# Kernel tuning notes

Hardware: AMD Instinct MI355X
Metric: run time of the kernel (lower is better)

The kernel has to match this reference:

```python
import jax, jax.numpy as jnp
import numpy as np

N = 100000     # nodes
E = 1600000    # directed edges
IN, HID, OUT = 128, 64, 64


def setup_inputs() -> dict:
    key = jax.random.key(0)
    k = jax.random.split(key, 6)
    features = jax.random.normal(k[0], (N, IN), dtype=jnp.float32)
    edge_index = jax.random.randint(k[1], (2, E), 0, N, dtype=jnp.int64)
    # Glorot-ish init for linear weights, zeros for bias (PyG GCNConv default)
    W1 = jax.random.normal(k[2], (IN, HID), dtype=jnp.float32) / np.sqrt(IN)
    b1 = jnp.zeros((HID,), dtype=jnp.float32)
    W2 = jax.random.normal(k[3], (HID, OUT), dtype=jnp.float32) / np.sqrt(HID)
    b2 = jnp.zeros((OUT,), dtype=jnp.float32)
    return {"features": features, "edge_index": edge_index, "batch_size": N,
            "W1": W1, "b1": b1, "W2": W2, "b2": b2}


def _gcn_conv(x, W, b, src, dst, n):
    """PyG GCNConv: add self-loops, symmetric deg^-1/2 normalization,
    linear transform then scatter-add aggregation, plus bias."""
    loops = jnp.arange(n, dtype=src.dtype)
    s = jnp.concatenate([src, loops])   # [E+N]
    d = jnp.concatenate([dst, loops])   # [E+N]
    deg = jax.ops.segment_sum(jnp.ones(s.shape, dtype=x.dtype), d, num_segments=n)
    dinv = jnp.where(deg > 0, jax.lax.rsqrt(deg), jnp.zeros_like(deg))
    norm = dinv[s] * dinv[d]            # [E+N]
    h = x @ W                           # [n, out] transform before aggregation
    msg = h[s] * norm[:, None]          # gather + scale  [E+N, out]
    out = jax.ops.segment_sum(msg, d, num_segments=n)  # scatter-add
    return out + b


def reference(features, edge_index, batch_size, W1, b1, W2, b2):
    src, dst = edge_index[0], edge_index[1]
    n = features.shape[0]
    x = _gcn_conv(features, W1, b1, src, dst, n)
    x = jax.nn.relu(x)
    # F.dropout(training=self.training): module is in eval mode -> identity
    x = _gcn_conv(x, W2, b2, src, dst, n)
    return jax.nn.log_softmax(x, axis=1)
```

## Files before the change

### kernel.cpp

```cpp
#include <hip/hip_runtime.h>
#include <math.h>

#define K1 128
#define C  64
#define SCAN_B 1024

__global__ void detect_kernel(const int* __restrict__ e, int twoE, int* __restrict__ flag) {
    __shared__ int nz;
    if (threadIdx.x == 0) nz = 0;
    __syncthreads();
    int nchk = twoE / 2; if (nchk > 4096) nchk = 4096;
    int bad = 0;
    for (int i = threadIdx.x; i < nchk; i += blockDim.x)
        if (e[2 * i + 1] != 0) bad = 1;
    if (bad) atomicOr(&nz, 1);
    __syncthreads();
    if (threadIdx.x == 0) *flag = nz ? 0 : 1;
}

__global__ void convert_kernel(const void* __restrict__ ein, int twoE,
                               const int* __restrict__ flag, int* __restrict__ eout) {
    int is64 = *flag;
    int i = blockIdx.x * blockDim.x + threadIdx.x;
    int stride = gridDim.x * blockDim.x;
    if (is64) {
        const long long* p = (const long long*)ein;
        for (; i < twoE; i += stride) eout[i] = (int)p[i];
    } else {
        const int* p = (const int*)ein;
        for (; i < twoE; i += stride) eout[i] = p[i];
    }
}

__global__ void zero_kernel(int* __restrict__ p, int n) {
    for (int i = blockIdx.x * blockDim.x + threadIdx.x; i < n; i += gridDim.x * blockDim.x)
        p[i] = 0;
}

__global__ void cnt_kernel(const int* __restrict__ dst, int E, int* __restrict__ cnt) {
    for (int e = blockIdx.x * blockDim.x + threadIdx.x; e < E; e += gridDim.x * blockDim.x)
        atomicAdd(&cnt[dst[e]], 1);
}

__global__ void dinv_kernel(const int* __restrict__ cnt, float* __restrict__ dinv, int n) {
    for (int i = blockIdx.x * blockDim.x + threadIdx.x; i < n; i += gridDim.x * blockDim.x)
        dinv[i] = rsqrtf((float)(cnt[i] + 1));
}

__global__ __launch_bounds__(SCAN_B) void scan1_kernel(const int* __restrict__ cnt, int n,
        int* __restrict__ ex, int* __restrict__ bsum) {
    __shared__ int s[SCAN_B];
    int i = blockIdx.x * SCAN_B + threadIdx.x;
    int v = (i < n) ? cnt[i] : 0;
    s[threadIdx.x] = v;
    __syncthreads();
    for (int off = 1; off < SCAN_B; off <<= 1) {
        int t = (threadIdx.x >= off) ? s[threadIdx.x - off] : 0;
        __syncthreads();
        s[threadIdx.x] += t;
        __syncthreads();
    }
    if (i < n) ex[i] = s[threadIdx.x] - v;
    if (threadIdx.x == SCAN_B - 1) bsum[blockIdx.x] = s[SCAN_B - 1];
}

__global__ void scan2_kernel(int* __restrict__ bsum, int nb) {
    const int lane = threadIdx.x & 63;
    int acc = 0;
    for (int base = 0; base < nb; base += 64) {
        int v = (base + lane < nb) ? bsum[base + lane] : 0;
        int sc = v;
        #pragma unroll
        for (int off = 1; off < 64; off <<= 1) {
            int t = __shfl_up(sc, off, 64);
            if (lane >= off) sc += t;
        }
        if (base + lane < nb) bsum[base + lane] = acc + sc - v;
        acc += __shfl(sc, 63, 64);
    }
}

__global__ void scan3_kernel(int* __restrict__ ex, const int* __restrict__ bsum,
                             int* __restrict__ fill, int n, int Etot) {
    for (int i = blockIdx.x * blockDim.x + threadIdx.x; i < n; i += gridDim.x * blockDim.x) {
        int v = ex[i] + bsum[i / SCAN_B];
        ex[i] = v;
        fill[i] = v;
    }
    if (blockIdx.x == 0 && threadIdx.x == 0) ex[n] = Etot;
}

__global__ void scatter_kernel(const int* __restrict__ src, const int* __restrict__ dst,
                               int E, int* __restrict__ fill, int* __restrict__ csr) {
    for (int e = blockIdx.x * blockDim.x + threadIdx.x; e < E; e += gridDim.x * blockDim.x) {
        int pos = atomicAdd(&fill[dst[e]], 1);
        csr[pos] = src[e];
    }
}

template<int K, int R>
__global__ __launch_bounds__(256) void gemm_kernel(const float* __restrict__ X,
        const float* __restrict__ W, const float* __restrict__ dinv,
        float* __restrict__ G, int n)
{
    __shared__ float Ws[K * C];
    for (int i = threadIdx.x; i < K * C; i += 256) Ws[i] = W[i];
    __syncthreads();
    const int lane = threadIdx.x & 63;
    const int wave = __builtin_amdgcn_readfirstlane((int)(threadIdx.x >> 6));
    const int waves = gridDim.x * 4;
    for (int base = (blockIdx.x * 4 + wave) * R; base < n; base += waves * R) {
        float acc[R];
        #pragma unroll
        for (int r = 0; r < R; ++r) acc[r] = 0.0f;
        if (base + R <= n) {
            for (int k = 0; k < K; ++k) {
                float w = Ws[k * C + lane];
                #pragma unroll
                for (int r = 0; r < R; ++r)
                    acc[r] = fmaf(X[(size_t)(base + r) * K + k], w, acc[r]);
            }
            #pragma unroll
            for (int r = 0; r < R; ++r)
                G[(size_t)(base + r) * C + lane] = acc[r] * dinv[base + r];
        } else {
            for (int r = 0; r < R; ++r) {
                if (base + r >= n) break;
                float a = 0.0f;
                for (int k = 0; k < K; ++k)
                    a = fmaf(X[(size_t)(base + r) * K + k], Ws[k * C + lane], a);
                G[(size_t)(base + r) * C + lane] = a * dinv[base + r];
            }
        }
    }
}

template<int MODE>
__global__ __launch_bounds__(256) void gather_kernel(const int* __restrict__ rowptr,
        const int* __restrict__ csr, const float* __restrict__ G,
        const float* __restrict__ dinv, const float* __restrict__ bias,
        float* __restrict__ Out, int n)
{
    const int lane = threadIdx.x & 63;
    const int v = __builtin_amdgcn_readfirstlane((int)(blockIdx.x * 4 + (threadIdx.x >> 6)));
    if (v >= n) return;
    const int start = __builtin_amdgcn_readfirstlane(rowptr[v]);
    const int end   = __builtin_amdgcn_readfirstlane(rowptr[v + 1]);
    float a0 = G[(size_t)v * C + lane];
    float a1 = 0.f, a2 = 0.f, a3 = 0.f;
    for (int base = start; base < end; base += 64) {
        int m = end - base; if (m > 64) m = 64;
        int idx = (lane < m) ? csr[base + lane] : 0;
        int j = 0;
        for (; j + 4 <= m; j += 4) {
            int s0 = __shfl(idx, j,     64);
            int s1 = __shfl(idx, j + 1, 64);
            int s2 = __shfl(idx, j + 2, 64);
            int s3 = __shfl(idx, j + 3, 64);
            a0 += G[(size_t)s0 * C + lane];
            a1 += G[(size_t)s1 * C + lane];
            a2 += G[(size_t)s2 * C + lane];
            a3 += G[(size_t)s3 * C + lane];
        }
        for (; j < m; ++j) {
            int s = __shfl(idx, j, 64);
            a0 += G[(size_t)s * C + lane];
        }
    }
    float acc = (a0 + a1) + (a2 + a3);
    float y = fmaf(acc, dinv[v], bias[lane]);
    if (MODE == 0) {
        Out[(size_t)v * C + lane] = y > 0.f ? y : 0.f;
    } else {
        float mx = y;
        #pragma unroll
        for (int off = 32; off > 0; off >>= 1) mx = fmaxf(mx, __shfl_xor(mx, off, 64));
        float ex = expf(y - mx);
        float l = ex;
        #pragma unroll
        for (int off = 32; off > 0; off >>= 1) l += __shfl_xor(l, off, 64);
        Out[(size_t)v * C + lane] = y - mx - logf(l);
    }
}

static inline size_t align16(size_t x) { return (x + 15) & ~(size_t)15; }

extern "C" void kernel_launch(void* const* d_in, const int* in_sizes, int n_in,
                              void* d_out, int out_size, void* d_ws, size_t ws_size,
                              hipStream_t stream)
{
    const float* X  = (const float*)d_in[0];
    const void*  EI = d_in[1];
    const float* W1 = (const float*)d_in[3];
    const float* b1 = (const float*)d_in[4];
    const float* W2 = (const float*)d_in[5];
    const float* b2 = (const float*)d_in[6];
    float* Out = (float*)d_out;

    const int n    = in_sizes[0] / K1;
    const int E    = in_sizes[1] / 2;
    const int twoE = 2 * E;
    const int nb   = (n + SCAN_B - 1) / SCAN_B;

    char* ws = (char*)d_ws;
    size_t off = 0;
    int*   edges  = (int*)(ws + off); off = align16(off + (size_t)twoE * 4);
    int*   csr    = (int*)(ws + off); off = align16(off + (size_t)E * 4);
    int*   rowptr = (int*)(ws + off); off = align16(off + (size_t)(n + 1) * 4);
    int*   cnt    = (int*)(ws + off); off = align16(off + (size_t)n * 4);
    int*   bsum   = (int*)(ws + off); off = align16(off + (size_t)(nb + 1) * 4);
    int*   flag   = (int*)(ws + off); off = align16(off + 16);
    float* dinv   = (float*)(ws + off); off = align16(off + (size_t)n * 4);
    float* G      = (float*)(ws + off); off = align16(off + (size_t)n * C * 4);
    int*   fill   = cnt;
    float* H      = Out;

    const int* srcp = edges;
    const int* dstp = edges + E;

    hipLaunchKernelGGL(detect_kernel,  dim3(1),    dim3(256), 0, stream, (const int*)EI, twoE, flag);
    hipLaunchKernelGGL(convert_kernel, dim3(4096), dim3(256), 0, stream, EI, twoE, flag, edges);

    hipLaunchKernelGGL(zero_kernel, dim3(512),  dim3(256), 0, stream, cnt, n);
    hipLaunchKernelGGL(cnt_kernel,  dim3(2048), dim3(256), 0, stream, dstp, E, cnt);
    hipLaunchKernelGGL(dinv_kernel, dim3(512),  dim3(256), 0, stream, cnt, dinv, n);
    hipLaunchKernelGGL(scan1_kernel, dim3(nb), dim3(SCAN_B), 0, stream, cnt, n, rowptr, bsum);
    hipLaunchKernelGGL(scan2_kernel, dim3(1),  dim3(64),     0, stream, bsum, nb);
    hipLaunchKernelGGL(scan3_kernel, dim3(1024), dim3(256),  0, stream, rowptr, bsum, fill, n, E);
    hipLaunchKernelGGL(scatter_kernel, dim3(2048), dim3(256), 0, stream, srcp, dstp, E, fill, csr);

    const int ngb = (n + 3) / 4;

    hipLaunchKernelGGL((gemm_kernel<K1, 8>), dim3(2048), dim3(256), 0, stream, X, W1, dinv, G, n);
    hipLaunchKernelGGL((gather_kernel<0>), dim3(ngb), dim3(256), 0, stream, rowptr, csr, G, dinv, b1, H, n);

    hipLaunchKernelGGL((gemm_kernel<C, 8>), dim3(2048), dim3(256), 0, stream, H, W2, dinv, G, n);
    hipLaunchKernelGGL((gather_kernel<1>), dim3(ngb), dim3(256), 0, stream, rowptr, csr, G, dinv, b2, Out, n);
}
```

Before: 583.4 us.

## Fuse layer-2 GEMM into gather, store features in fp16, drop edge conversion

Removes the edge int64-to-int32 conversion pass by reading edge_index directly in the histogram and scatter kernels. The degree-inverse computation moves into the scan kernel, and a memset replaces the zero kernel. The transformed features G are now stored as fp16, halving the bytes moved by the random-gather aggregation. The layer-1 aggregation is fused with ReLU and the layer-2 64x64 transform, which drops a full GEMM pass and the H round-trip, at the cost of 64 registers of W2 per thread and reduced-precision intermediates.

```diff
diff --git a/kernel.cpp b/kernel.cpp
--- a/kernel.cpp
+++ b/kernel.cpp
@@ -1,4 +1,5 @@
 #include <hip/hip_runtime.h>
+#include <hip/hip_fp16.h>
 #include <math.h>
 
 #define K1 128
@@ -18,37 +19,22 @@
     if (threadIdx.x == 0) *flag = nz ? 0 : 1;
 }
 
-__global__ void convert_kernel(const void* __restrict__ ein, int twoE,
-                               const int* __restrict__ flag, int* __restrict__ eout) {
-    int is64 = *flag;
-    int i = blockIdx.x * blockDim.x + threadIdx.x;
-    int stride = gridDim.x * blockDim.x;
-    if (is64) {
-        const long long* p = (const long long*)ein;
-        for (; i < twoE; i += stride) eout[i] = (int)p[i];
-    } else {
-        const int* p = (const int*)ein;
-        for (; i < twoE; i += stride) eout[i] = p[i];
-    }
-}
-
-__global__ void zero_kernel(int* __restrict__ p, int n) {
-    for (int i = blockIdx.x * blockDim.x + threadIdx.x; i < n; i += gridDim.x * blockDim.x)
-        p[i] = 0;
-}
-
-__global__ void cnt_kernel(const int* __restrict__ dst, int E, int* __restrict__ cnt) {
-    for (int e = blockIdx.x * blockDim.x + threadIdx.x; e < E; e += gridDim.x * blockDim.x)
-        atomicAdd(&cnt[dst[e]], 1);
-}
-
-__global__ void dinv_kernel(const int* __restrict__ cnt, float* __restrict__ dinv, int n) {
-    for (int i = blockIdx.x * blockDim.x + threadIdx.x; i < n; i += gridDim.x * blockDim.x)
-        dinv[i] = rsqrtf((float)(cnt[i] + 1));
+__device__ __forceinline__ int load_dst(const void* EI, int E, int e, int is64) {
+    return is64 ? (int)((const long long*)EI)[(size_t)E + e] : ((const int*)EI)[(size_t)E + e];
+}
+__device__ __forceinline__ int load_src(const void* EI, int E, int e, int is64) {
+    return is64 ? (int)((const long long*)EI)[e] : ((const int*)EI)[e];
+}
+
+__global__ __launch_bounds__(256) void hist_kernel(const void* __restrict__ EI, int E,
+        const int* __restrict__ flag, int* __restrict__ cnt) {
+    const int is64 = *flag;
+    for (int e = blockIdx.x * 256 + threadIdx.x; e < E; e += gridDim.x * 256)
+        atomicAdd(&cnt[load_dst(EI, E, e, is64)], 1);
 }
 
 __global__ __launch_bounds__(SCAN_B) void scan1_kernel(const int* __restrict__ cnt, int n,
-        int* __restrict__ ex, int* __restrict__ bsum) {
+        int* __restrict__ ex, int* __restrict__ bsum, float* __restrict__ dinv) {
     __shared__ int s[SCAN_B];
     int i = blockIdx.x * SCAN_B + threadIdx.x;
     int v = (i < n) ? cnt[i] : 0;
@@ -60,7 +46,10 @@
         s[threadIdx.x] += t;
         __syncthreads();
     }
-    if (i < n) ex[i] = s[threadIdx.x] - v;
+    if (i < n) {
+        ex[i] = s[threadIdx.x] - v;
+        dinv[i] = rsqrtf((float)(v + 1));
+    }
     if (threadIdx.x == SCAN_B - 1) bsum[blockIdx.x] = s[SCAN_B - 1];
 }
 
@@ -90,18 +79,21 @@
     if (blockIdx.x == 0 && threadIdx.x == 0) ex[n] = Etot;
 }
 
-__global__ void scatter_kernel(const int* __restrict__ src, const int* __restrict__ dst,
-                               int E, int* __restrict__ fill, int* __restrict__ csr) {
-    for (int e = blockIdx.x * blockDim.x + threadIdx.x; e < E; e += gridDim.x * blockDim.x) {
-        int pos = atomicAdd(&fill[dst[e]], 1);
-        csr[pos] = src[e];
+__global__ __launch_bounds__(256) void scatter_kernel(const void* __restrict__ EI, int E,
+        const int* __restrict__ flag, int* __restrict__ fill, int* __restrict__ csr) {
+    const int is64 = *flag;
+    for (int e = blockIdx.x * 256 + threadIdx.x; e < E; e += gridDim.x * 256) {
+        int d = load_dst(EI, E, e, is64);
+        int s = load_src(EI, E, e, is64);
+        int pos = atomicAdd(&fill[d], 1);
+        csr[pos] = s;
     }
 }
 
 template<int K, int R>
 __global__ __launch_bounds__(256) void gemm_kernel(const float* __restrict__ X,
         const float* __restrict__ W, const float* __restrict__ dinv,
-        float* __restrict__ G, int n)
+        __half* __restrict__ G, int n)
 {
     __shared__ float Ws[K * C];
     for (int i = threadIdx.x; i < K * C; i += 256) Ws[i] = W[i];
@@ -122,22 +114,74 @@
             }
             #pragma unroll
             for (int r = 0; r < R; ++r)
-                G[(size_t)(base + r) * C + lane] = acc[r] * dinv[base + r];
+                G[(size_t)(base + r) * C + lane] = __float2half_rn(acc[r] * dinv[base + r]);
         } else {
             for (int r = 0; r < R; ++r) {
                 if (base + r >= n) break;
                 float a = 0.0f;
                 for (int k = 0; k < K; ++k)
                     a = fmaf(X[(size_t)(base + r) * K + k], Ws[k * C + lane], a);
-                G[(size_t)(base + r) * C + lane] = a * dinv[base + r];
-            }
-        }
-    }
-}
-
-template<int MODE>
-__global__ __launch_bounds__(256) void gather_kernel(const int* __restrict__ rowptr,
-        const int* __restrict__ csr, const float* __restrict__ G,
+                G[(size_t)(base + r) * C + lane] = __float2half_rn(a * dinv[base + r]);
+            }
+        }
+    }
+}
+
+__global__ __launch_bounds__(256) void gather_fused_kernel(const int* __restrict__ rowptr,
+        const int* __restrict__ csr, const __half* __restrict__ G,
+        const float* __restrict__ dinv, const float* __restrict__ b1,
+        const float* __restrict__ W2, __half* __restrict__ G2, int n)
+{
+    __shared__ __align__(16) float Hrow[4][C];
+    const int lane = threadIdx.x & 63;
+    const int wv = __builtin_amdgcn_readfirstlane((int)(threadIdx.x >> 6));
+    float w[C];
+    #pragma unroll
+    for (int k = 0; k < C; ++k) w[k] = W2[k * C + lane];
+    const float bias = b1[lane];
+    const int nwaves = gridDim.x * 4;
+    for (int v = __builtin_amdgcn_readfirstlane(blockIdx.x * 4 + wv); v < n; v += nwaves) {
+        const int start = __builtin_amdgcn_readfirstlane(rowptr[v]);
+        const int end   = __builtin_amdgcn_readfirstlane(rowptr[v + 1]);
+        float a0 = __half2float(G[(size_t)v * C + lane]);
+        float a1 = 0.f, a2 = 0.f, a3 = 0.f;
+        for (int base = start; base < end; base += 64) {
+            int m = end - base; if (m > 64) m = 64;
+            int idx = (lane < m) ? csr[base + lane] : 0;
+            int j = 0;
+            for (; j + 4 <= m; j += 4) {
+                int s0 = __shfl(idx, j,     64);
+                int s1 = __shfl(idx, j + 1, 64);
+                int s2 = __shfl(idx, j + 2, 64);
+                int s3 = __shfl(idx, j + 3, 64);
+                a0 += __half2float(G[(size_t)s0 * C + lane]);
+                a1 += __half2float(G[(size_t)s1 * C + lane]);
+                a2 += __half2float(G[(size_t)s2 * C + lane]);
+                a3 += __half2float(G[(size_t)s3 * C + lane]);
+            }
+            for (; j < m; ++j) {
+                int s = __shfl(idx, j, 64);
+                a0 += __half2float(G[(size_t)s * C + lane]);
+            }
+        }
+        float y = fmaf((a0 + a1) + (a2 + a3), dinv[v], bias);
+        y = y > 0.f ? y : 0.f;
+        Hrow[wv][lane] = y;
+        float o = 0.f;
+        #pragma unroll
+        for (int k0 = 0; k0 < C / 4; ++k0) {
+            float4 h4 = *(const float4*)&Hrow[wv][k0 * 4];
+            o = fmaf(h4.x, w[4 * k0 + 0], o);
+            o = fmaf(h4.y, w[4 * k0 + 1], o);
+            o = fmaf(h4.z, w[4 * k0 + 2], o);
+            o = fmaf(h4.w, w[4 * k0 + 3], o);
+        }
+        G2[(size_t)v * C + lane] = __float2half_rn(o * dinv[v]);
+    }
+}
+
+__global__ __launch_bounds__(256) void gather_ls_kernel(const int* __restrict__ rowptr,
+        const int* __restrict__ csr, const __half* __restrict__ G,
         const float* __restrict__ dinv, const float* __restrict__ bias,
         float* __restrict__ Out, int n)
 {
@@ -146,7 +190,7 @@
     if (v >= n) return;
     const int start = __builtin_amdgcn_readfirstlane(rowptr[v]);
     const int end   = __builtin_amdgcn_readfirstlane(rowptr[v + 1]);
-    float a0 = G[(size_t)v * C + lane];
+    float a0 = __half2float(G[(size_t)v * C + lane]);
     float a1 = 0.f, a2 = 0.f, a3 = 0.f;
     for (int base = start; base < end; base += 64) {
         int m = end - base; if (m > 64) m = 64;
@@ -157,30 +201,25 @@
             int s1 = __shfl(idx, j + 1, 64);
             int s2 = __shfl(idx, j + 2, 64);
             int s3 = __shfl(idx, j + 3, 64);
-            a0 += G[(size_t)s0 * C + lane];
-            a1 += G[(size_t)s1 * C + lane];
-            a2 += G[(size_t)s2 * C + lane];
-            a3 += G[(size_t)s3 * C + lane];
+            a0 += __half2float(G[(size_t)s0 * C + lane]);
+            a1 += __half2float(G[(size_t)s1 * C + lane]);
+            a2 += __half2float(G[(size_t)s2 * C + lane]);
+            a3 += __half2float(G[(size_t)s3 * C + lane]);
         }
         for (; j < m; ++j) {
             int s = __shfl(idx, j, 64);
-            a0 += G[(size_t)s * C + lane];
-        }
-    }
-    float acc = (a0 + a1) + (a2 + a3);
-    float y = fmaf(acc, dinv[v], bias[lane]);
-    if (MODE == 0) {
-        Out[(size_t)v * C + lane] = y > 0.f ? y : 0.f;
-    } else {
-        float mx = y;
-        #pragma unroll
-        for (int off = 32; off > 0; off >>= 1) mx = fmaxf(mx, __shfl_xor(mx, off, 64));
-        float ex = expf(y - mx);
-        float l = ex;
-        #pragma unroll
-        for (int off = 32; off > 0; off >>= 1) l += __shfl_xor(l, off, 64);
-        Out[(size_t)v * C + lane] = y - mx - logf(l);
-    }
+            a0 += __half2float(G[(size_t)s * C + lane]);
+        }
+    }
+    float y = fmaf((a0 + a1) + (a2 + a3), dinv[v], bias[lane]);
+    float mx = y;
+    #pragma unroll
+    for (int off = 32; off > 0; off >>= 1) mx = fmaxf(mx, __shfl_xor(mx, off, 64));
+    float ex = expf(y - mx);
+    float l = ex;
+    #pragma unroll
+    for (int off = 32; off > 0; off >>= 1) l += __shfl_xor(l, off, 64);
+    Out[(size_t)v * C + lane] = y - mx - logf(l);
 }
 
 static inline size_t align16(size_t x) { return (x + 15) & ~(size_t)15; }
@@ -204,36 +243,29 @@
 
     char* ws = (char*)d_ws;
     size_t off = 0;
-    int*   edges  = (int*)(ws + off); off = align16(off + (size_t)twoE * 4);
-    int*   csr    = (int*)(ws + off); off = align16(off + (size_t)E * 4);
-    int*   rowptr = (int*)(ws + off); off = align16(off + (size_t)(n + 1) * 4);
-    int*   cnt    = (int*)(ws + off); off = align16(off + (size_t)n * 4);
-    int*   bsum   = (int*)(ws + off); off = align16(off + (size_t)(nb + 1) * 4);
-    int*   flag   = (int*)(ws + off); off = align16(off + 16);
-    float* dinv   = (float*)(ws + off); off = align16(off + (size_t)n * 4);
-    float* G      = (float*)(ws + off); off = align16(off + (size_t)n * C * 4);
-    int*   fill   = cnt;
-    float* H      = Out;
-
-    const int* srcp = edges;
-    const int* dstp = edges + E;
-
-    hipLaunchKernelGGL(detect_kernel,  dim3(1),    dim3(256), 0, stream, (const int*)EI, twoE, flag);
-    hipLaunchKernelGGL(convert_kernel, dim3(4096), dim3(256), 0, stream, EI, twoE, flag, edges);
-
-    hipLaunchKernelGGL(zero_kernel, dim3(512),  dim3(256), 0, stream, cnt, n);
-    hipLaunchKernelGGL(cnt_kernel,  dim3(2048), dim3(256), 0, stream, dstp, E, cnt);
-    hipLaunchKernelGGL(dinv_kernel, dim3(512),  dim3(256), 0, stream, cnt, dinv, n);
-    hipLaunchKernelGGL(scan1_kernel, dim3(nb), dim3(SCAN_B), 0, stream, cnt, n, rowptr, bsum);
-    hipLaunchKernelGGL(scan2_kernel, dim3(1),  dim3(64),     0, stream, bsum, nb);
-    hipLaunchKernelGGL(scan3_kernel, dim3(1024), dim3(256),  0, stream, rowptr, bsum, fill, n, E);
-    hipLaunchKernelGGL(scatter_kernel, dim3(2048), dim3(256), 0, stream, srcp, dstp, E, fill, csr);
-
+    int*    csr    = (int*)(ws + off);    off = align16(off + (size_t)E * 4);
+    int*    rowptr = (int*)(ws + off);    off = align16(off + (size_t)(n + 1) * 4);
+    int*    cnt    = (int*)(ws + off);    off = align16(off + (size_t)n * 4);
+    int*    bsum   = (int*)(ws + off);    off = align16(off + (size_t)(nb + 1) * 4);
+    int*    flag   = (int*)(ws + off);    off = align16(off + 16);
+    float*  dinv   = (float*)(ws + off);  off = align16(off + (size_t)n * 4);
+    __half* G      = (__half*)(ws + off); off = align16(off + (size_t)n * C * 2);
+    __half* G2     = (__half*)(ws + off); off = align16(off + (size_t)n * C * 2);
+    int*    fill   = cnt;
+
+    hipLaunchKernelGGL(detect_kernel, dim3(1), dim3(256), 0, stream, (const int*)EI, twoE, flag);
+    hipMemsetAsync(cnt, 0, (size_t)n * 4, stream);
+
+    hipLaunchKernelGGL(hist_kernel,  dim3(1024), dim3(256), 0, stream, EI, E, flag, cnt);
+    hipLaunchKernelGGL(scan1_kernel, dim3(nb), dim3(SCAN_B), 0, stream, cnt, n, rowptr, bsum, dinv);
+    hipLaunchKernelGGL(scan2_kernel, dim3(1), dim3(64), 0, stream, bsum, nb);
+    hipLaunchKernelGGL(scan3_kernel, dim3(1024), dim3(256), 0, stream, rowptr, bsum, fill, n, E);
+    hipLaunchKernelGGL(scatter_kernel, dim3(2048), dim3(256), 0, stream, EI, E, flag, fill, csr);
+
+    hipLaunchKernelGGL((gemm_kernel<K1, 8>), dim3(2048), dim3(256), 0, stream, X, W1, dinv, G, n);
+    hipLaunchKernelGGL(gather_fused_kernel, dim3(2048), dim3(256), 0, stream,
+                       rowptr, csr, G, dinv, b1, W2, G2, n);
     const int ngb = (n + 3) / 4;
-
-    hipLaunchKernelGGL((gemm_kernel<K1, 8>), dim3(2048), dim3(256), 0, stream, X, W1, dinv, G, n);
-    hipLaunchKernelGGL((gather_kernel<0>), dim3(ngb), dim3(256), 0, stream, rowptr, csr, G, dinv, b1, H, n);
-
-    hipLaunchKernelGGL((gemm_kernel<C, 8>), dim3(2048), dim3(256), 0, stream, H, W2, dinv, G, n);
-    hipLaunchKernelGGL((gather_kernel<1>), dim3(ngb), dim3(256), 0, stream, rowptr, csr, G, dinv, b2, Out, n);
-}
+    hipLaunchKernelGGL(gather_ls_kernel, dim3(ngb), dim3(256), 0, stream,
+                       rowptr, csr, G2, dinv, b2, Out, n);
+}
```

Result: faster. 524.7 us (-10.1%).
